# Kernel optimization log

Measured on AMD Instinct MI355X. Metric: run time of the kernel, lower is better.

The kernel has to match this reference:

```python
import jax, jax.numpy as jnp
import numpy as np

B, C1, C2, H, L, D, NC = 32, 256, 256, 64, 40, 768, 8
SIGMA_W = 0.1
EMB = (D + NC * 2) // 2  # 392


def _conv(x, w, scale, shift, pad):
    # ultralytics-style Conv: conv2d(bias=False) + eval-mode BN (folded into per-channel
    # scale/shift) + SiLU activation
    y = jax.lax.conv_general_dilated(x, w, (1, 1), [(pad, pad), (pad, pad)],
                                     dimension_numbers=('NCHW', 'OIHW', 'NCHW'))
    y = y * scale[None, :, None, None] + shift[None, :, None, None]
    return y * jax.nn.sigmoid(y)  # SiLU


def _l2norm(x, eps=1e-12):
    n = jnp.sqrt(jnp.sum(x * x, axis=1, keepdims=True))
    return x / jnp.maximum(n, eps)


def setup_inputs() -> dict:
    key = jax.random.key(0)
    ks = jax.random.split(key, 20)
    img = jax.random.normal(ks[0], (B, C1, H, H), jnp.float32)
    flang = jax.random.normal(ks[1], (B, L, D), jnp.float32)
    # contiguous valid mask with >=3 tokens (CLS + >=1 word + SEP)
    lens = jax.random.randint(ks[2], (B,), 3, L + 1)
    word_mask = (jnp.arange(L)[None, :] < lens[:, None]).astype(jnp.int32)
    p = lambda k, s: jax.random.normal(k, s, jnp.float32) * 0.02
    return {
        'img': img, 'flang': flang, 'word_mask': word_mask,
        'w_visu': p(ks[3], (C2, C1, 1, 1)), 's_visu': jnp.ones((C2,)), 'b_visu': jnp.zeros((C2,)),
        'w_g': p(ks[4], (NC, NC, 1, 1)), 's_g': jnp.ones((NC,)), 'b_g': jnp.zeros((NC,)),
        'w_b': p(ks[5], (NC, NC, 1, 1)), 's_b': jnp.ones((NC,)), 'b_b': jnp.zeros((NC,)),
        'W1': p(ks[6], (EMB, D)), 'b1': jnp.zeros((EMB,)),
        'W2': p(ks[7], (2 * NC, EMB)), 'b2': jnp.zeros((2 * NC,)),
        'w_f1': p(ks[8], (C1, C1, 1, 1)), 's_f1': jnp.ones((C1,)), 'b_f1': jnp.zeros((C1,)),
        'w_f2': p(ks[9], (C1, C1, 3, 3)), 's_f2': jnp.ones((C1,)), 'b_f2': jnp.zeros((C1,)),
        'w_f3': p(ks[10], (C2, C1, 1, 1)), 'bias_f3': jnp.zeros((C2,)),
        'add_weight': jnp.zeros((), jnp.float32),
    }


def reference(img, flang, word_mask, w_visu, s_visu, b_visu, w_g, s_g, b_g,
              w_b, s_b, b_b, W1, b1, W2, b2, w_f1, s_f1, b_f1, w_f2, s_f2, b_f2,
              w_f3, bias_f3, add_weight):
    height = img.shape[2]
    # mapping_visu: Conv 1x1 + BN + SiLU, then tanh
    map_visu = jnp.tanh(_conv(img, w_visu, s_visu, b_visu, 0))  # [B,C2,H,H]

    # vectorized get_avg_flang: mean over selected tokens excluding first and last selected
    m = word_mask.astype(jnp.int32)
    csum = jnp.cumsum(m, axis=1)                     # [B,L]
    total = csum[:, -1:]
    inner = ((m == 1) & (csum > 1) & (csum < total)).astype(flang.dtype)  # [B,L]
    cnt = jnp.sum(inner, axis=1, keepdims=True)
    flang_avg = jnp.sum(flang * inner[:, :, None], axis=1) / cnt  # [B,D]

    # mapping_lang: two stacked Linears (no activation between), then sigmoid
    h = flang_avg @ W1.T + b1
    map_flang = jax.nn.sigmoid(h @ W2.T + b2)        # [B,2*NC]
    maps = map_flang.reshape(-1, NC, 2)

    sigma = SIGMA_W * height
    yc = (maps[:, :, 0] * height).astype(jnp.int32)[:, :, None, None]
    xc = (maps[:, :, 1] * height).astype(jnp.int32)[:, :, None, None]
    gy, gx = jnp.meshgrid(jnp.arange(height), jnp.arange(height), indexing='ij')
    gy = gy[None, None]; gx = gx[None, None]
    d2 = ((gy - yc) ** 2 + (gx - xc) ** 2).astype(jnp.float32)
    weights = jnp.exp(-d2 / (2.0 * sigma ** 2))      # [B,NC,H,H]

    gamma = jnp.tanh(_conv(weights, w_g, s_g, b_g, 0))
    beta = jnp.tanh(_conv(weights, w_b, s_b, b_b, 0))
    g = jnp.mean(gamma, axis=1, keepdims=True)       # [B,1,H,H]
    b = jnp.max(beta, axis=1, keepdims=True)         # [B,1,H,H]

    v_film = _l2norm(g * map_visu + b)               # [B,C2,H,H]
    # mapping_fusion: Conv1x1 -> Conv3x3 -> plain Conv2d 1x1 with bias
    v = _conv(v_film, w_f1, s_f1, b_f1, 0)
    v = _conv(v, w_f2, s_f2, b_f2, 1)
    v_film = jax.lax.conv_general_dilated(v, w_f3, (1, 1), [(0, 0), (0, 0)],
                                          dimension_numbers=('NCHW', 'OIHW', 'NCHW'))
    v_film = v_film + bias_f3[None, :, None, None]

    add_w = jnp.tanh(add_weight)
    v_add = (1.0 + add_w) * img + (1.0 - add_w) * v_film
    return _l2norm(v_add)
```

## Files before the change

kernel.cpp:

```cpp
#include <hip/hip_runtime.h>
#include <hip/hip_bf16.h>

#define B_   32
#define C_   256
#define HH   64
#define P_   4096
#define L_   40
#define D_   768
#define NC_  8
#define EMB_ 392
#define CP_  (C_*P_)
#define LOS  264

typedef __attribute__((ext_vector_type(8))) short bf16x8;
typedef __attribute__((ext_vector_type(4))) float f32x4;
typedef unsigned short u16;

static __device__ __forceinline__ float siluf(float y) {
    return y / (1.f + expf(-y));
}
static __device__ __forceinline__ u16 f2b(float f) {
    __hip_bfloat16 h = __float2bfloat16(f);
    return *reinterpret_cast<u16*>(&h);
}
static __device__ __forceinline__ float b2f(u16 u) {
    unsigned v = ((unsigned)u) << 16;
    return __int_as_float((int)v);
}
static __device__ __forceinline__ int swz(int row, int col) {
    int ch = (col >> 3) ^ ((row & 7) << 2);
    return row * 256 + ch * 8 + (col & 7);
}

typedef __attribute__((address_space(1))) const unsigned int g_u32;
typedef __attribute__((address_space(3))) unsigned int l_u32;
static __device__ __forceinline__ void gl_lds(const u16* g, short* l) {
    __builtin_amdgcn_global_load_lds((g_u32*)g, (l_u32*)l, 16, 0, 0);
}
#define VMCNT6() asm volatile("s_waitcnt vmcnt(6)" ::: "memory")
#define VMCNT0() asm volatile("s_waitcnt vmcnt(0)" ::: "memory")
#define RBAR()  do { __builtin_amdgcn_s_barrier(); __builtin_amdgcn_sched_barrier(0); } while (0)

__global__ __launch_bounds__(256) void k_prep(
    const float* __restrict__ wv, const float* __restrict__ wf1,
    const float* __restrict__ wf3, const float* __restrict__ wf2,
    u16* __restrict__ WV, u16* __restrict__ WF1,
    u16* __restrict__ WF3, u16* __restrict__ WF2, u16* __restrict__ zblk)
{
    int i = blockIdx.x * 256 + threadIdx.x;
    int oc = i >> 8, ic = i & 255;
    WV[i]  = f2b(wv[i]);
    WF1[i] = f2b(wf1[i]);
    WF3[i] = f2b(wf3[i]);
#pragma unroll
    for (int tap = 0; tap < 9; ++tap)
        WF2[oc * 2304 + tap * 256 + ic] = f2b(wf2[oc * 2304 + ic * 9 + tap]);
    if (blockIdx.x == 0 && threadIdx.x < 16) zblk[threadIdx.x] = 0;
}

__global__ __launch_bounds__(256) void k_imgT(
    const float* __restrict__ img, u16* __restrict__ imgT)
{
    int b = blockIdx.z, pix0 = blockIdx.x * 32, ic0 = blockIdx.y * 32;
    int t = threadIdx.x;
    __shared__ float T[32][33];
    int ic = t >> 3, ps = (t & 7) * 4;
    f32x4 v = *(const f32x4*)&img[((size_t)b * C_ + ic0 + ic) * P_ + pix0 + ps];
    T[ic][ps] = v[0]; T[ic][ps + 1] = v[1]; T[ic][ps + 2] = v[2]; T[ic][ps + 3] = v[3];
    __syncthreads();
    int px = t >> 3, sg = (t & 7) * 4;
    u16 o0 = f2b(T[sg + 0][px]), o1 = f2b(T[sg + 1][px]);
    u16 o2 = f2b(T[sg + 2][px]), o3 = f2b(T[sg + 3][px]);
    uint2 val;
    val.x = (unsigned)o0 | ((unsigned)o1 << 16);
    val.y = (unsigned)o2 | ((unsigned)o3 << 16);
    *(uint2*)(imgT + ((size_t)b * P_ + pix0 + px) * C_ + ic0 + sg) = val;
}

__global__ __launch_bounds__(256) void k_lang(
    const float* __restrict__ flang, const int* __restrict__ wmask,
    const float* __restrict__ W1, const float* __restrict__ b1,
    const float* __restrict__ W2, const float* __restrict__ b2,
    int* __restrict__ centers)
{
    int b = blockIdx.x, tid = threadIdx.x;
    __shared__ float inner[L_];
    __shared__ float cnt_s;
    __shared__ float favg[D_];
    __shared__ float hbuf[EMB_];
    __shared__ float mfs[16];

    if (tid == 0) {
        int total = 0;
        for (int l = 0; l < L_; ++l) total += wmask[b * L_ + l];
        int c = 0, cntv = 0;
        for (int l = 0; l < L_; ++l) {
            int m = wmask[b * L_ + l];
            c += m;
            float f = (m == 1 && c > 1 && c < total) ? 1.f : 0.f;
            inner[l] = f;
            cntv += (f != 0.f);
        }
        cnt_s = (float)cntv;
    }
    __syncthreads();
    float cinv = 1.f / cnt_s;
    for (int d = tid; d < D_; d += 256) {
        float s = 0.f;
        for (int l = 0; l < L_; ++l)
            s += flang[((size_t)b * L_ + l) * D_ + d] * inner[l];
        favg[d] = s * cinv;
    }
    __syncthreads();
    for (int e = tid; e < EMB_; e += 256) {
        float s = b1[e];
        const float* w = W1 + (size_t)e * D_;
        for (int d = 0; d < D_; ++d) s += w[d] * favg[d];
        hbuf[e] = s;
    }
    __syncthreads();
    if (tid < 16) {
        float s = b2[tid];
        const float* w = W2 + tid * EMB_;
        for (int d = 0; d < EMB_; ++d) s += w[d] * hbuf[d];
        mfs[tid] = 1.f / (1.f + expf(-s));
    }
    __syncthreads();
    if (tid < NC_) {
        centers[b * (NC_ * 2) + tid * 2 + 0] = (int)(mfs[tid * 2 + 0] * (float)HH);
        centers[b * (NC_ * 2) + tid * 2 + 1] = (int)(mfs[tid * 2 + 1] * (float)HH);
    }
}

__global__ __launch_bounds__(256) void k_gb(
    const int* __restrict__ centers,
    const float* __restrict__ wg, const float* __restrict__ sg, const float* __restrict__ bg,
    const float* __restrict__ wb, const float* __restrict__ sb, const float* __restrict__ bb,
    float* __restrict__ gmap, float* __restrict__ bmap)
{
    int idx = blockIdx.x * 256 + threadIdx.x;
    int b = idx >> 12;
    int p = idx & 4095;
    int gy = p >> 6, gx = p & 63;

    float w[NC_];
#pragma unroll
    for (int nc = 0; nc < NC_; ++nc) {
        int yc = centers[b * (NC_ * 2) + nc * 2 + 0];
        int xc = centers[b * (NC_ * 2) + nc * 2 + 1];
        int dy = gy - yc, dx = gx - xc;
        w[nc] = expf(-(float)(dy * dy + dx * dx) / 81.92f);
    }
    float gsum = 0.f, bmx = -1e30f;
#pragma unroll
    for (int c = 0; c < NC_; ++c) {
        float ag = 0.f, ab = 0.f;
#pragma unroll
        for (int ic = 0; ic < NC_; ++ic) {
            ag += wg[c * NC_ + ic] * w[ic];
            ab += wb[c * NC_ + ic] * w[ic];
        }
        gsum += tanhf(siluf(sg[c] * ag + bg[c]));
        bmx = fmaxf(bmx, tanhf(siluf(sb[c] * ab + bb[c])));
    }
    gmap[idx] = gsum * (1.f / (float)NC_);
    bmap[idx] = bmx;
}

static __device__ __forceinline__ void frag_load(const short* sA, const short* sW,
                                                 int l15, int qa, int w,
                                                 bf16x8 a[8], bf16x8 bb[4])
{
#pragma unroll
    for (int m = 0; m < 8; ++m)
        a[m] = *(const bf16x8*)&sA[(m * 16 + l15) * 32 + qa * 8];
#pragma unroll
    for (int n = 0; n < 4; ++n)
        bb[n] = *(const bf16x8*)&sW[(w * 64 + n * 16 + l15) * 32 + qa * 8];
}
static __device__ __forceinline__ void frag_compute(const bf16x8 a[8], const bf16x8 bb[4],
                                                    f32x4 acc[8][4])
{
#pragma unroll
    for (int m = 0; m < 8; ++m)
#pragma unroll
        for (int n = 0; n < 4; ++n)
            acc[m][n] = __builtin_amdgcn_mfma_f32_16x16x32_bf16(a[m], bb[n], acc[m][n], 0, 0, 0);
}

__global__ __launch_bounds__(256, 2) void k_vf1(
    const u16* __restrict__ X, const u16* __restrict__ WV, const u16* __restrict__ WF1,
    const float* __restrict__ s_visu, const float* __restrict__ b_visu,
    const float* __restrict__ gmap, const float* __restrict__ bmap,
    const float* __restrict__ s_f1, const float* __restrict__ b_f1,
    u16* __restrict__ Y)
{
    int b = blockIdx.y, p0 = blockIdx.x * 128, t = threadIdx.x;
    int lane = t & 63, w = t >> 6;
    int l15 = t & 15, q = (t >> 4) & 3;
    int qa = q ^ ((l15 >> 1) & 3);
    int lc = (lane & 3) ^ ((lane >> 3) & 3);
    int lp = lane >> 2;
    __shared__ __align__(16) short LO[32768];
    __shared__ __align__(16) short W2[8192];
    float* red  = (float*)W2;
    float* invs = (float*)(W2 + 1024);
    const u16* Xb = X + (size_t)b * CP_;

    f32x4 acc[8][4];
#pragma unroll
    for (int m = 0; m < 8; ++m)
#pragma unroll
        for (int n = 0; n < 4; ++n) acc[m][n] = (f32x4)0.f;

    auto stage1 = [&](int s, int buf) {
        int k0 = s * 32;
        short* bA = LO + buf * 12288;
        short* bW = bA + 4096;
#pragma unroll
        for (int i = 0; i < 2; ++i) {
            int pr = (w * 2 + i) * 16 + lp;
            gl_lds(Xb + (size_t)(p0 + pr) * C_ + k0 + lc * 8, bA + (w * 2 + i) * 512);
        }
#pragma unroll
        for (int j = 0; j < 4; ++j) {
            int oc = (w * 4 + j) * 16 + lp;
            gl_lds(WV + (size_t)oc * 256 + k0 + lc * 8, bW + (w * 4 + j) * 512);
        }
    };
    stage1(0, 0);
    VMCNT0();
    __syncthreads();
    for (int s = 0; s < 8; ++s) {
        int cur = s & 1;
        bf16x8 a[8], bb[4];
        frag_load(LO + cur * 12288, LO + cur * 12288 + 4096, l15, qa, w, a, bb);
        if (s < 7) stage1(s + 1, cur ^ 1);
        frag_compute(a, bb, acc);
        VMCNT0();
        __syncthreads();
    }

    {
        float sc[4], sh[4];
#pragma unroll
        for (int n = 0; n < 4; ++n) {
            int oc = w * 64 + n * 16 + l15;
            sc[n] = s_visu[oc]; sh[n] = b_visu[oc];
        }
#pragma unroll
        for (int m = 0; m < 8; ++m) {
            f32x4 gv = *(const f32x4*)&gmap[(size_t)b * P_ + p0 + m * 16 + q * 4];
            f32x4 bm = *(const f32x4*)&bmap[(size_t)b * P_ + p0 + m * 16 + q * 4];
            float ps[4] = {0.f, 0.f, 0.f, 0.f};
#pragma unroll
            for (int n = 0; n < 4; ++n)
#pragma unroll
                for (int r = 0; r < 4; ++r) {
                    float y = sc[n] * acc[m][n][r] + sh[n];
                    float v = gv[r] * tanhf(siluf(y)) + bm[r];
                    acc[m][n][r] = v;
                    ps[r] += v * v;
                }
#pragma unroll
            for (int r = 0; r < 4; ++r) {
                float p = ps[r];
                p += __shfl_xor(p, 1);
                p += __shfl_xor(p, 2);
                p += __shfl_xor(p, 4);
                p += __shfl_xor(p, 8);
                if (l15 == 0) red[w * 128 + m * 16 + q * 4 + r] = p;
            }
        }
    }
    __syncthreads();
    if (t < 128) {
        float s = red[0 * 128 + t] + red[1 * 128 + t] + red[2 * 128 + t] + red[3 * 128 + t];
        invs[t] = 1.f / fmaxf(sqrtf(s), 1e-12f);
    }
    __syncthreads();

#pragma unroll
    for (int m = 0; m < 8; ++m) {
        f32x4 iv = *(const f32x4*)&invs[m * 16 + q * 4];
#pragma unroll
        for (int n = 0; n < 4; ++n)
#pragma unroll
            for (int r = 0; r < 4; ++r) {
                int row = m * 16 + q * 4 + r;
                int col = w * 64 + n * 16 + l15;
                LO[swz(row, col)] = (short)f2b(acc[m][n][r] * iv[r]);
            }
    }
    __syncthreads();

#pragma unroll
    for (int m = 0; m < 8; ++m)
#pragma unroll
        for (int n = 0; n < 4; ++n) acc[m][n] = (f32x4)0.f;

    for (int ks = 0; ks < 8; ++ks) {
#pragma unroll
        for (int j = 0; j < 4; ++j) {
            int oc = (w * 4 + j) * 16 + lp;
            gl_lds(WF1 + (size_t)oc * 256 + ks * 32 + lc * 8, W2 + (w * 4 + j) * 512);
        }
        VMCNT0();
        __syncthreads();
        bf16x8 a[8], bb[4];
#pragma unroll
        for (int m = 0; m < 8; ++m) {
            int row = m * 16 + l15;
            int ch = (ks * 4 + q) ^ ((row & 7) << 2);
            a[m] = *(const bf16x8*)&LO[row * 256 + ch * 8];
        }
#pragma unroll
        for (int n = 0; n < 4; ++n)
            bb[n] = *(const bf16x8*)&W2[(w * 64 + n * 16 + l15) * 32 + qa * 8];
        frag_compute(a, bb, acc);
        __syncthreads();
    }

    {
        float sc[4], sh[4];
#pragma unroll
        for (int n = 0; n < 4; ++n) {
            int oc = w * 64 + n * 16 + l15;
            sc[n] = s_f1[oc]; sh[n] = b_f1[oc];
        }
        __syncthreads();
#pragma unroll
        for (int m = 0; m < 8; ++m)
#pragma unroll
            for (int n = 0; n < 4; ++n)
#pragma unroll
                for (int r = 0; r < 4; ++r) {
                    int row = m * 16 + q * 4 + r;
                    int col = w * 64 + n * 16 + l15;
                    LO[swz(row, col)] = (short)f2b(siluf(sc[n] * acc[m][n][r] + sh[n]));
                }
    }
    __syncthreads();
    u16* Yb = Y + (size_t)b * CP_ + (size_t)p0 * C_;
#pragma unroll
    for (int h = 0; h < 2; ++h) {
        int row = h * 64 + (t >> 2);
        u16* dp = Yb + (size_t)row * C_;
#pragma unroll
        for (int u = 0; u < 8; ++u) {
            int ch = (t & 3) + u * 4;
            int sc_ = ch ^ ((row & 7) << 2);
            *(uint4*)(dp + ch * 8) = *(const uint4*)&LO[row * 256 + sc_ * 8];
        }
    }
}

__global__ __launch_bounds__(256, 2) void k_f2(
    const u16* __restrict__ X, const u16* __restrict__ W,
    const float* __restrict__ scale, const float* __restrict__ shift,
    const u16* __restrict__ zblk, u16* __restrict__ Y)
{
    int b = blockIdx.y, p0 = blockIdx.x * 128, t = threadIdx.x;
    int lane = t & 63, w = t >> 6;
    int l15 = t & 15, q = (t >> 4) & 3;
    int qa = q ^ ((l15 >> 1) & 3);
    int lc = (lane & 3) ^ ((lane >> 3) & 3);
    int lp = lane >> 2;
    __shared__ __align__(16) short SM[3 * 12288];
    const u16* Xb = X + (size_t)b * CP_;

    f32x4 acc[8][4];
#pragma unroll
    for (int m = 0; m < 8; ++m)
#pragma unroll
        for (int n = 0; n < 4; ++n) acc[m][n] = (f32x4)0.f;

    auto stage = [&](int s, int buf) {
        int k0 = s * 32;
        int tap = s >> 3;
        int icb = (s & 7) * 32;
        int dy = tap / 3 - 1, dx = tap - (tap / 3) * 3 - 1;
        short* bA = SM + buf * 12288;
        short* bW = bA + 4096;
#pragma unroll
        for (int i = 0; i < 2; ++i) {
            int pr = (w * 2 + i) * 16 + lp;
            int p = p0 + pr;
            int y = (p >> 6) + dy, x = (p & 63) + dx;
            const u16* gp = ((unsigned)y < (unsigned)HH && (unsigned)x < (unsigned)HH)
                ? Xb + (size_t)(y * HH + x) * C_ + icb + lc * 8
                : zblk;
            gl_lds(gp, bA + (w * 2 + i) * 512);
        }
#pragma unroll
        for (int j = 0; j < 4; ++j) {
            int oc = (w * 4 + j) * 16 + lp;
            gl_lds(W + (size_t)oc * 2304 + k0 + lc * 8, bW + (w * 4 + j) * 512);
        }
    };

    stage(0, 0);
    stage(1, 1);
    VMCNT6();
    RBAR();
    for (int s = 0; s < 72; ++s) {
        int cur = s % 3;
        bf16x8 a[8], bb[4];
        frag_load(SM + cur * 12288, SM + cur * 12288 + 4096, l15, qa, w, a, bb);
        if (s < 70) stage(s + 2, (s + 2) % 3);
        frag_compute(a, bb, acc);
        if (s < 70) { VMCNT6(); } else { VMCNT0(); }
        RBAR();
    }

    float sc[4], sh[4];
#pragma unroll
    for (int n = 0; n < 4; ++n) {
        int oc = w * 64 + n * 16 + l15;
        sc[n] = scale[oc]; sh[n] = shift[oc];
    }
    short* LO = SM;
#pragma unroll
    for (int m = 0; m < 8; ++m)
#pragma unroll
        for (int n = 0; n < 4; ++n)
#pragma unroll
            for (int r = 0; r < 4; ++r) {
                float v = siluf(sc[n] * acc[m][n][r] + sh[n]);
                LO[(m * 16 + q * 4 + r) * LOS + w * 64 + n * 16 + l15] = (short)f2b(v);
            }
    __syncthreads();

    u16* Yb = Y + (size_t)b * CP_ + (size_t)p0 * C_;
#pragma unroll
    for (int h = 0; h < 2; ++h) {
        int row = h * 64 + (t >> 2);
        const short* sp = &LO[row * LOS];
        u16* dp = Yb + (size_t)row * C_;
#pragma unroll
        for (int u = 0; u < 8; ++u) {
            int c = (t & 3) * 8 + u * 32;
            *(uint4*)(dp + c) = *(const uint4*)(sp + c);
        }
    }
}

__global__ __launch_bounds__(256, 2) void k_final(
    const u16* __restrict__ X, const u16* __restrict__ W,
    const float* __restrict__ bias_f3, const float* __restrict__ img,
    const float* __restrict__ add_w, float* __restrict__ out)
{
    int b = blockIdx.y, p0 = blockIdx.x * 128, t = threadIdx.x;
    int lane = t & 63, w = t >> 6;
    int l15 = t & 15, q = (t >> 4) & 3;
    int qa = q ^ ((l15 >> 1) & 3);
    int lc = (lane & 3) ^ ((lane >> 3) & 3);
    int lp = lane >> 2;
    __shared__ __align__(16) short SM[2 * 12288];
    __shared__ float red[4][128];
    __shared__ float invs[128];
    const u16* Xb = X + (size_t)b * CP_;

    f32x4 acc[8][4];
#pragma unroll
    for (int m = 0; m < 8; ++m)
#pragma unroll
        for (int n = 0; n < 4; ++n) acc[m][n] = (f32x4)0.f;

    auto stage = [&](int s, int buf) {
        int k0 = s * 32;
        short* bA = SM + buf * 12288;
        short* bW = bA + 4096;
#pragma unroll
        for (int i = 0; i < 2; ++i) {
            int pr = (w * 2 + i) * 16 + lp;
            gl_lds(Xb + (size_t)(p0 + pr) * C_ + k0 + lc * 8, bA + (w * 2 + i) * 512);
        }
#pragma unroll
        for (int j = 0; j < 4; ++j) {
            int oc = (w * 4 + j) * 16 + lp;
            gl_lds(W + (size_t)oc * 256 + k0 + lc * 8, bW + (w * 4 + j) * 512);
        }
    };

    stage(0, 0);
    VMCNT0();
    __syncthreads();
    for (int s = 0; s < 8; ++s) {
        int cur = s & 1;
        bf16x8 a[8], bb[4];
        frag_load(SM + cur * 12288, SM + cur * 12288 + 4096, l15, qa, w, a, bb);
        if (s < 7) stage(s + 1, cur ^ 1);
        frag_compute(a, bb, acc);
        VMCNT0();
        __syncthreads();
    }

    float aw = tanhf(add_w[0]);
    float c1 = 1.f + aw, c2 = 1.f - aw;
    float bf[4];
#pragma unroll
    for (int n = 0; n < 4; ++n) bf[n] = bias_f3[w * 64 + n * 16 + l15];

#pragma unroll
    for (int m = 0; m < 8; ++m) {
        float ps[4] = {0.f, 0.f, 0.f, 0.f};
#pragma unroll
        for (int n = 0; n < 4; ++n) {
            int oc = w * 64 + n * 16 + l15;
            f32x4 iv = *(const f32x4*)&img[((size_t)b * C_ + oc) * P_ + p0 + m * 16 + q * 4];
#pragma unroll
            for (int r = 0; r < 4; ++r) {
                float v = c1 * iv[r] + c2 * (acc[m][n][r] + bf[n]);
                acc[m][n][r] = v;
                ps[r] += v * v;
            }
        }
#pragma unroll
        for (int r = 0; r < 4; ++r) {
            float p = ps[r];
            p += __shfl_xor(p, 1);
            p += __shfl_xor(p, 2);
            p += __shfl_xor(p, 4);
            p += __shfl_xor(p, 8);
            if (l15 == 0) red[w][m * 16 + q * 4 + r] = p;
        }
    }
    __syncthreads();
    if (t < 128) {
        float s = red[0][t] + red[1][t] + red[2][t] + red[3][t];
        invs[t] = 1.f / fmaxf(sqrtf(s), 1e-12f);
    }
    __syncthreads();
#pragma unroll
    for (int m = 0; m < 8; ++m) {
        f32x4 iv = *(const f32x4*)&invs[m * 16 + q * 4];
#pragma unroll
        for (int n = 0; n < 4; ++n) {
            int oc = w * 64 + n * 16 + l15;
            f32x4 o;
#pragma unroll
            for (int r = 0; r < 4; ++r) o[r] = acc[m][n][r] * iv[r];
            *(f32x4*)&out[((size_t)b * C_ + oc) * P_ + p0 + m * 16 + q * 4] = o;
        }
    }
}

extern "C" void kernel_launch(void* const* d_in, const int* in_sizes, int n_in,
                              void* d_out, int out_size, void* d_ws, size_t ws_size,
                              hipStream_t stream)
{
    const float* img     = (const float*)d_in[0];
    const float* flang   = (const float*)d_in[1];
    const int*   wmask   = (const int*)d_in[2];
    const float* w_visu  = (const float*)d_in[3];
    const float* s_visu  = (const float*)d_in[4];
    const float* b_visu  = (const float*)d_in[5];
    const float* w_g     = (const float*)d_in[6];
    const float* s_g     = (const float*)d_in[7];
    const float* b_g     = (const float*)d_in[8];
    const float* w_b     = (const float*)d_in[9];
    const float* s_b     = (const float*)d_in[10];
    const float* b_b     = (const float*)d_in[11];
    const float* W1      = (const float*)d_in[12];
    const float* b1      = (const float*)d_in[13];
    const float* W2      = (const float*)d_in[14];
    const float* b2      = (const float*)d_in[15];
    const float* w_f1    = (const float*)d_in[16];
    const float* s_f1    = (const float*)d_in[17];
    const float* b_f1    = (const float*)d_in[18];
    const float* w_f2    = (const float*)d_in[19];
    const float* s_f2    = (const float*)d_in[20];
    const float* b_f2    = (const float*)d_in[21];
    const float* w_f3    = (const float*)d_in[22];
    const float* bias_f3 = (const float*)d_in[23];
    const float* add_w   = (const float*)d_in[24];

    float* out = (float*)d_out;

    u16* bigA = (u16*)d_ws;
    u16* bigB = bigA + (size_t)B_ * CP_;
    u16* WV   = bigB + (size_t)B_ * CP_;
    u16* WF1  = WV + 65536;
    u16* WF3  = WF1 + 65536;
    u16* WF2  = WF3 + 65536;
    float* gmap = (float*)(WF2 + 589824);
    float* bmap = gmap + (size_t)B_ * P_;
    int* centers = (int*)(bmap + (size_t)B_ * P_);
    u16* zblk = (u16*)(centers + 512);

    k_prep<<<256, 256, 0, stream>>>(w_visu, w_f1, w_f3, w_f2, WV, WF1, WF3, WF2, zblk);
    k_lang<<<B_, 256, 0, stream>>>(flang, wmask, W1, b1, W2, b2, centers);
    k_gb<<<(B_ * P_) / 256, 256, 0, stream>>>(centers, w_g, s_g, b_g, w_b, s_b, b_b, gmap, bmap);
    k_imgT<<<dim3(P_ / 32, C_ / 32, B_), 256, 0, stream>>>(img, bigB);
    k_vf1<<<dim3(P_ / 128, B_), 256, 0, stream>>>(bigB, WV, WF1, s_visu, b_visu,
                                                  gmap, bmap, s_f1, b_f1, bigB);
    k_f2<<<dim3(P_ / 128, B_), 256, 0, stream>>>(bigB, WF2, s_f2, b_f2, zblk, bigA);
    k_final<<<dim3(P_ / 128, B_), 256, 0, stream>>>(bigA, WF3, bias_f3, img, add_w, out);
}
```

Baseline: 507.9 us.

## Load GEMM fragments directly from global and reuse halo tile for 3x3 conv

The 1x1 conv kernels (k_vf1, k_final) drop LDS staging and read MFMA fragments straight from global memory. This removes barriers and async copies but relies on L1/L2 for reuse. The 3x3 conv kernel switches from per-tap implicit-GEMM staging to loading a haloed 4-row input tile into LDS once per 32-channel chunk. All nine taps are then computed from that tile, with weights read directly from global. The aim is to cut redundant input loads across taps, at the cost of uncoalesced global fragment loads and less latency hiding.

```diff
diff --git a/kernel.cpp b/kernel.cpp
--- a/kernel.cpp
+++ b/kernel.cpp
@@ -37,9 +37,7 @@
 static __device__ __forceinline__ void gl_lds(const u16* g, short* l) {
     __builtin_amdgcn_global_load_lds((g_u32*)g, (l_u32*)l, 16, 0, 0);
 }
-#define VMCNT6() asm volatile("s_waitcnt vmcnt(6)" ::: "memory")
 #define VMCNT0() asm volatile("s_waitcnt vmcnt(0)" ::: "memory")
-#define RBAR()  do { __builtin_amdgcn_s_barrier(); __builtin_amdgcn_sched_barrier(0); } while (0)
 
 __global__ __launch_bounds__(256) void k_prep(
     const float* __restrict__ wv, const float* __restrict__ wf1,
@@ -167,17 +165,6 @@
     bmap[idx] = bmx;
 }
 
-static __device__ __forceinline__ void frag_load(const short* sA, const short* sW,
-                                                 int l15, int qa, int w,
-                                                 bf16x8 a[8], bf16x8 bb[4])
-{
-#pragma unroll
-    for (int m = 0; m < 8; ++m)
-        a[m] = *(const bf16x8*)&sA[(m * 16 + l15) * 32 + qa * 8];
-#pragma unroll
-    for (int n = 0; n < 4; ++n)
-        bb[n] = *(const bf16x8*)&sW[(w * 64 + n * 16 + l15) * 32 + qa * 8];
-}
 static __device__ __forceinline__ void frag_compute(const bf16x8 a[8], const bf16x8 bb[4],
                                                     f32x4 acc[8][4])
 {
@@ -196,15 +183,11 @@
     u16* __restrict__ Y)
 {
     int b = blockIdx.y, p0 = blockIdx.x * 128, t = threadIdx.x;
-    int lane = t & 63, w = t >> 6;
+    int w = t >> 6;
     int l15 = t & 15, q = (t >> 4) & 3;
-    int qa = q ^ ((l15 >> 1) & 3);
-    int lc = (lane & 3) ^ ((lane >> 3) & 3);
-    int lp = lane >> 2;
     __shared__ __align__(16) short LO[32768];
-    __shared__ __align__(16) short W2[8192];
-    float* red  = (float*)W2;
-    float* invs = (float*)(W2 + 1024);
+    __shared__ float red[4][128];
+    __shared__ float invs[128];
     const u16* Xb = X + (size_t)b * CP_;
 
     f32x4 acc[8][4];
@@ -213,32 +196,15 @@
 #pragma unroll
         for (int n = 0; n < 4; ++n) acc[m][n] = (f32x4)0.f;
 
-    auto stage1 = [&](int s, int buf) {
-        int k0 = s * 32;
-        short* bA = LO + buf * 12288;
-        short* bW = bA + 4096;
-#pragma unroll
-        for (int i = 0; i < 2; ++i) {
-            int pr = (w * 2 + i) * 16 + lp;
-            gl_lds(Xb + (size_t)(p0 + pr) * C_ + k0 + lc * 8, bA + (w * 2 + i) * 512);
-        }
-#pragma unroll
-        for (int j = 0; j < 4; ++j) {
-            int oc = (w * 4 + j) * 16 + lp;
-            gl_lds(WV + (size_t)oc * 256 + k0 + lc * 8, bW + (w * 4 + j) * 512);
-        }
-    };
-    stage1(0, 0);
-    VMCNT0();
-    __syncthreads();
-    for (int s = 0; s < 8; ++s) {
-        int cur = s & 1;
+    for (int ks = 0; ks < 8; ++ks) {
         bf16x8 a[8], bb[4];
-        frag_load(LO + cur * 12288, LO + cur * 12288 + 4096, l15, qa, w, a, bb);
-        if (s < 7) stage1(s + 1, cur ^ 1);
+#pragma unroll
+        for (int n = 0; n < 4; ++n)
+            bb[n] = *(const bf16x8*)&WV[(size_t)(w * 64 + n * 16 + l15) * 256 + ks * 32 + q * 8];
+#pragma unroll
+        for (int m = 0; m < 8; ++m)
+            a[m] = *(const bf16x8*)&Xb[(size_t)(p0 + m * 16 + l15) * C_ + ks * 32 + q * 8];
         frag_compute(a, bb, acc);
-        VMCNT0();
-        __syncthreads();
     }
 
     {
@@ -269,13 +235,13 @@
                 p += __shfl_xor(p, 2);
                 p += __shfl_xor(p, 4);
                 p += __shfl_xor(p, 8);
-                if (l15 == 0) red[w * 128 + m * 16 + q * 4 + r] = p;
+                if (l15 == 0) red[w][m * 16 + q * 4 + r] = p;
             }
         }
     }
     __syncthreads();
     if (t < 128) {
-        float s = red[0 * 128 + t] + red[1 * 128 + t] + red[2 * 128 + t] + red[3 * 128 + t];
+        float s = red[0][t] + red[1][t] + red[2][t] + red[3][t];
         invs[t] = 1.f / fmaxf(sqrtf(s), 1e-12f);
     }
     __syncthreads();
@@ -300,25 +266,17 @@
         for (int n = 0; n < 4; ++n) acc[m][n] = (f32x4)0.f;
 
     for (int ks = 0; ks < 8; ++ks) {
-#pragma unroll
-        for (int j = 0; j < 4; ++j) {
-            int oc = (w * 4 + j) * 16 + lp;
-            gl_lds(WF1 + (size_t)oc * 256 + ks * 32 + lc * 8, W2 + (w * 4 + j) * 512);
-        }
-        VMCNT0();
-        __syncthreads();
         bf16x8 a[8], bb[4];
+#pragma unroll
+        for (int n = 0; n < 4; ++n)
+            bb[n] = *(const bf16x8*)&WF1[(size_t)(w * 64 + n * 16 + l15) * 256 + ks * 32 + q * 8];
 #pragma unroll
         for (int m = 0; m < 8; ++m) {
             int row = m * 16 + l15;
             int ch = (ks * 4 + q) ^ ((row & 7) << 2);
             a[m] = *(const bf16x8*)&LO[row * 256 + ch * 8];
         }
-#pragma unroll
-        for (int n = 0; n < 4; ++n)
-            bb[n] = *(const bf16x8*)&W2[(w * 64 + n * 16 + l15) * 32 + qa * 8];
         frag_compute(a, bb, acc);
-        __syncthreads();
     }
 
     {
@@ -363,10 +321,8 @@
     int b = blockIdx.y, p0 = blockIdx.x * 128, t = threadIdx.x;
     int lane = t & 63, w = t >> 6;
     int l15 = t & 15, q = (t >> 4) & 3;
-    int qa = q ^ ((l15 >> 1) & 3);
-    int lc = (lane & 3) ^ ((lane >> 3) & 3);
-    int lp = lane >> 2;
-    __shared__ __align__(16) short SM[3 * 12288];
+    int h0 = blockIdx.x * 2;
+    __shared__ __align__(16) short SM[128 * LOS];
     const u16* Xb = X + (size_t)b * CP_;
 
     f32x4 acc[8][4];
@@ -375,42 +331,50 @@
 #pragma unroll
         for (int n = 0; n < 4; ++n) acc[m][n] = (f32x4)0.f;
 
-    auto stage = [&](int s, int buf) {
-        int k0 = s * 32;
-        int tap = s >> 3;
-        int icb = (s & 7) * 32;
-        int dy = tap / 3 - 1, dx = tap - (tap / 3) * 3 - 1;
-        short* bA = SM + buf * 12288;
-        short* bW = bA + 4096;
-#pragma unroll
-        for (int i = 0; i < 2; ++i) {
-            int pr = (w * 2 + i) * 16 + lp;
-            int p = p0 + pr;
-            int y = (p >> 6) + dy, x = (p & 63) + dx;
-            const u16* gp = ((unsigned)y < (unsigned)HH && (unsigned)x < (unsigned)HH)
-                ? Xb + (size_t)(y * HH + x) * C_ + icb + lc * 8
-                : zblk;
-            gl_lds(gp, bA + (w * 2 + i) * 512);
-        }
-#pragma unroll
-        for (int j = 0; j < 4; ++j) {
-            int oc = (w * 4 + j) * 16 + lp;
-            gl_lds(W + (size_t)oc * 2304 + k0 + lc * 8, bW + (w * 4 + j) * 512);
+    {
+        int buf = (t >> 7) & 1, r = (t >> 5) & 3, bd = (t >> 4) & 1, icp = t & 15;
+        *(unsigned*)&SM[buf * 8448 + r * 2112 + bd * 2080 + icp * 2] = 0u;
+    }
+
+    auto stageA = [&](int cc, int buf) {
+        int y = h0 - 1 + w;
+        bool ok = (unsigned)y < (unsigned)HH;
+        short* dst0 = SM + buf * 8448 + w * 2112 + 32;
+        const u16* rowbase = Xb + (size_t)y * HH * C_ + cc * 32;
+#pragma unroll
+        for (int g = 0; g < 4; ++g) {
+            const u16* src = ok ? (rowbase + (size_t)(g * 16 + (lane >> 2)) * C_ + (lane & 3) * 8)
+                                : zblk;
+            gl_lds(src, dst0 + g * 512);
         }
     };
 
-    stage(0, 0);
-    stage(1, 1);
-    VMCNT6();
-    RBAR();
-    for (int s = 0; s < 72; ++s) {
-        int cur = s % 3;
-        bf16x8 a[8], bb[4];
-        frag_load(SM + cur * 12288, SM + cur * 12288 + 4096, l15, qa, w, a, bb);
-        if (s < 70) stage(s + 2, (s + 2) % 3);
-        frag_compute(a, bb, acc);
-        if (s < 70) { VMCNT6(); } else { VMCNT0(); }
-        RBAR();
+    stageA(0, 0);
+    VMCNT0();
+    __syncthreads();
+
+    for (int cc = 0; cc < 8; ++cc) {
+        int buf = cc & 1;
+        if (cc < 7) stageA(cc + 1, buf ^ 1);
+        const short* Ah = SM + buf * 8448;
+#pragma unroll
+        for (int tap = 0; tap < 9; ++tap) {
+            int dy = tap / 3 - 1, dx = tap % 3 - 1;
+            bf16x8 a[8], bb[4];
+#pragma unroll
+            for (int n = 0; n < 4; ++n)
+                bb[n] = *(const bf16x8*)&W[(size_t)(w * 64 + n * 16 + l15) * 2304
+                                           + tap * 256 + cc * 32 + q * 8];
+#pragma unroll
+            for (int m = 0; m < 8; ++m) {
+                int row_l = (m >> 2) + 1 + dy;
+                int x_s = (m & 3) * 16 + l15 + dx + 1;
+                a[m] = *(const bf16x8*)&Ah[row_l * 2112 + x_s * 32 + q * 8];
+            }
+            frag_compute(a, bb, acc);
+        }
+        VMCNT0();
+        __syncthreads();
     }
 
     float sc[4], sh[4];
@@ -451,12 +415,8 @@
     const float* __restrict__ add_w, float* __restrict__ out)
 {
     int b = blockIdx.y, p0 = blockIdx.x * 128, t = threadIdx.x;
-    int lane = t & 63, w = t >> 6;
+    int w = t >> 6;
     int l15 = t & 15, q = (t >> 4) & 3;
-    int qa = q ^ ((l15 >> 1) & 3);
-    int lc = (lane & 3) ^ ((lane >> 3) & 3);
-    int lp = lane >> 2;
-    __shared__ __align__(16) short SM[2 * 12288];
     __shared__ float red[4][128];
     __shared__ float invs[128];
     const u16* Xb = X + (size_t)b * CP_;
@@ -467,33 +427,15 @@
 #pragma unroll
         for (int n = 0; n < 4; ++n) acc[m][n] = (f32x4)0.f;
 
-    auto stage = [&](int s, int buf) {
-        int k0 = s * 32;
-        short* bA = SM + buf * 12288;
-        short* bW = bA + 4096;
-#pragma unroll
-        for (int i = 0; i < 2; ++i) {
-            int pr = (w * 2 + i) * 16 + lp;
-            gl_lds(Xb + (size_t)(p0 + pr) * C_ + k0 + lc * 8, bA + (w * 2 + i) * 512);
-        }
-#pragma unroll
-        for (int j = 0; j < 4; ++j) {
-            int oc = (w * 4 + j) * 16 + lp;
-            gl_lds(W + (size_t)oc * 256 + k0 + lc * 8, bW + (w * 4 + j) * 512);
-        }
-    };
-
-    stage(0, 0);
-    VMCNT0();
-    __syncthreads();
-    for (int s = 0; s < 8; ++s) {
-        int cur = s & 1;
+    for (int ks = 0; ks < 8; ++ks) {
         bf16x8 a[8], bb[4];
-        frag_load(SM + cur * 12288, SM + cur * 12288 + 4096, l15, qa, w, a, bb);
-        if (s < 7) stage(s + 1, cur ^ 1);
+#pragma unroll
+        for (int n = 0; n < 4; ++n)
+            bb[n] = *(const bf16x8*)&W[(size_t)(w * 64 + n * 16 + l15) * 256 + ks * 32 + q * 8];
+#pragma unroll
+        for (int m = 0; m < 8; ++m)
+            a[m] = *(const bf16x8*)&Xb[(size_t)(p0 + m * 16 + l15) * C_ + ks * 32 + q * 8];
         frag_compute(a, bb, acc);
-        VMCNT0();
-        __syncthreads();
     }
 
     float aw = tanhf(add_w[0]);
```

After: 585.5 us. 15.3% more time.
